# Performance work log

Measured on AMD Instinct MI355X. Metric: run time of the kernel, lower is better.

## Reference

```python
import jax, jax.numpy as jnp
import numpy as np

N_CLUSTER = 1
SIZE, RATIO = 32, 0.1


def _lin_mat(n_in, n_out):
    # bilinear, align_corners=True interpolation matrix [n_out, n_in]
    src = np.arange(n_out) * (n_in - 1) / (n_out - 1)
    lo = np.floor(src).astype(np.int64)
    hi = np.minimum(lo + 1, n_in - 1)
    w = (src - lo).astype(np.float32)
    M = np.zeros((n_out, n_in), np.float32)
    M[np.arange(n_out), lo] += 1.0 - w
    M[np.arange(n_out), hi] += w
    return jnp.asarray(M)


def setup_inputs() -> dict:
    key = jax.random.key(0)
    ks = jax.random.split(key, 5)
    B, D, H, W, C = 16, 128, 128, 128, 6
    inp = {
        "assp": jax.random.normal(ks[0], (B, D, H, W), jnp.float32),
        "cls_w": jax.random.normal(ks[1], (C, D), jnp.float32) * 0.05,
        "cls_b": jnp.zeros((C,), jnp.float32),
        "key_w": jax.random.normal(ks[2], (128, D), jnp.float32) * 0.05,
        "key_b": jnp.zeros((128,), jnp.float32),
        "query_w": jax.random.normal(ks[3], (C, 128, D), jnp.float32) * 0.05,
        "query_b": jnp.zeros((C, 128), jnp.float32),
    }
    rng = np.random.default_rng(0)
    idx = rng.permutation(SIZE * SIZE)[: int(SIZE * SIZE * RATIO)]  # 102 unique pixels
    inp["px"] = jnp.asarray(idx // SIZE, jnp.int32)
    inp["py"] = jnp.asarray(idx % SIZE, jnp.int32)
    return inp


def reference(assp, cls_w, cls_b, key_w, key_b, query_w, query_b, px, py):
    B, D, H, W = assp.shape
    C = cls_w.shape[0]
    # pseudo labels (torch.no_grad)
    feats = jax.lax.stop_gradient(assp)
    pseudo = jnp.einsum('bdhw,cd->bchw', feats, cls_w) + cls_b[None, :, None, None]
    mask = jnp.argmax(pseudo, axis=1)                      # [B,H,W]
    onehot = jax.nn.one_hot(mask, C, dtype=assp.dtype)      # [B,H,W,C]
    counts = onehot.sum((1, 2))                             # [B,C]
    sums = jnp.einsum('bdhw,bhwc->bcd', assp, onehot)       # masked class sums
    protoC = sums / (counts[..., None] + 1e-5)              # [B,C,D]
    protoC = jnp.where(counts[..., None] > 0, protoC, 0.0)  # zero_prototype fallback
    protos12 = jnp.broadcast_to(protoC[:, :, None, :], (B, C, 2, D)).reshape(B, 2 * C, D)

    # DomainTrain: gather sampled pixels, L2 dist to 12 prototypes, argmin, scatter replace
    feat_px = assp[:, :, px, py]                            # [B,D,Np]
    diff = protos12[:, :, None, :] - feat_px.transpose(0, 2, 1)[:, None, :, :]  # [B,12,Np,D]
    dist = jnp.linalg.norm(diff, axis=-1)                   # [B,12,Np]
    closest = jnp.argmin(dist, axis=1)                      # [B,Np]
    repl = jnp.take_along_axis(protos12, closest[..., None], axis=1)  # [B,Np,D]
    assp = assp.at[:, :, px, py].set(repl.transpose(0, 2, 1))
    protos4 = protos12.reshape(B, C, 2, D)

    # key / query attention
    keymap = jnp.einsum('bdhw,kd->bkhw', assp, key_w) + key_b[None, :, None, None]
    q = jnp.einsum('bijd,ikd->bijk', protos4, query_w) + query_b[None, :, None, :]  # [B,C,2,128]
    sim = jnp.einsum('bijk,bkhw->bijhw', q, keymap).reshape(B, 2 * C, H, W)
    simw = jax.nn.softmax(sim / (2 * C) * N_CLUSTER, axis=1).mean(axis=1)  # [B,H,W]

    weighted = assp * simw[:, None]
    x = jnp.einsum('bdhw,cd->bchw', weighted, cls_w) + cls_b[None, :, None, None]
    My = _lin_mat(H, 4 * H)
    Mx = _lin_mat(W, 4 * W)
    xup = jnp.einsum('Hh,bchw,Ww->bcHW', My, x, Mx)
    return xup
```

## Files before the change

### kernel.cpp

```cpp
#include <hip/hip_runtime.h>

namespace {

constexpr int B  = 16;
constexpr int D  = 128;
constexpr int C  = 6;
constexpr int H  = 128;
constexpr int W  = 128;
constexpr int HWC = H * W;
constexpr int HO = 512, WO = 512;
constexpr int TILE = 64;
constexpr int TPB  = 4;

__global__ __launch_bounds__(256) void k_fused(const float* __restrict__ assp,
                                               const float* __restrict__ cls_w,
                                               const float* __restrict__ cls_b,
                                               float* __restrict__ sums,
                                               int* __restrict__ counts,
                                               float* __restrict__ x) {
  __shared__ float tile[D * TILE];
  __shared__ float red[4 * C * TILE];
  __shared__ float ws[C * D];
  __shared__ float bs[C];

  const int t  = threadIdx.x;
  const int b  = blockIdx.y;
  for (int i = t; i < C * D; i += 256) ws[i] = cls_w[i];
  if (t < C) bs[t] = cls_b[t];

  const int lane = t & 63;
  const int wv   = t >> 6;
  const int d2b  = t & 127;
  const int h2b  = t >> 7;
  const int d1   = t >> 5;
  const int px2  = (t & 31) * 2;

  float acc2b[C] = {0.f, 0.f, 0.f, 0.f, 0.f, 0.f};
  int   cnt_run  = 0;

  const int hw_base = blockIdx.x * (TILE * TPB);
  const float* bbase = assp + ((size_t)b * D) * HWC + hw_base;

  float2 v[16];
#pragma unroll
  for (int j = 0; j < 16; ++j) {
    int d = d1 + 8 * j;
    v[j] = *(const float2*)(bbase + (size_t)d * HWC + px2);
  }

  __syncthreads();

  for (int it = 0; it < TPB; ++it) {
    const int hw0 = hw_base + it * TILE;

#pragma unroll
    for (int j = 0; j < 16; ++j) {
      int d = d1 + 8 * j;
      *(float2*)&tile[d * TILE + (px2 ^ (d & 62))] = v[j];
    }
    __syncthreads();

    if (it + 1 < TPB) {
      const float* nbase = bbase + (it + 1) * TILE;
#pragma unroll
      for (int j = 0; j < 16; ++j) {
        int d = d1 + 8 * j;
        v[j] = *(const float2*)(nbase + (size_t)d * HWC + px2);
      }
    }

    {
      float a[C] = {0.f, 0.f, 0.f, 0.f, 0.f, 0.f};
#pragma unroll
      for (int dd = 0; dd < 32; ++dd) {
        int d = wv * 32 + dd;
        float vv = tile[d * TILE + (lane ^ (d & 62))];
#pragma unroll
        for (int c = 0; c < C; ++c) a[c] += vv * ws[c * D + d];
      }
#pragma unroll
      for (int c = 0; c < C; ++c) red[(wv * C + c) * TILE + lane] = a[c];
    }
    __syncthreads();

    int cls;
    {
      float s[C];
#pragma unroll
      for (int c = 0; c < C; ++c)
        s[c] = red[(0 * C + c) * TILE + lane] + red[(1 * C + c) * TILE + lane]
             + red[(2 * C + c) * TILE + lane] + red[(3 * C + c) * TILE + lane];
      float bv = s[0] + bs[0]; cls = 0;
#pragma unroll
      for (int c = 1; c < C; ++c) {
        float pv = s[c] + bs[c];
        if (pv > bv) { bv = pv; cls = c; }
      }
      if (wv == 0) {
        const float inv12 = 1.0f / 12.0f;
        float* xb = x + ((size_t)b * C) * HWC + hw0 + lane;
#pragma unroll
        for (int c = 0; c < C; ++c) xb[(size_t)c * HWC] = s[c] * inv12 + bs[c];
#pragma unroll
        for (int c = 0; c < C; ++c) {
          unsigned long long m = __ballot(cls == c);
          if (lane == c) cnt_run += (int)__popcll(m);
        }
      }
    }

#pragma unroll
    for (int i = 0; i < 32; ++i) {
      int px = h2b * 32 + i;
      float vv = tile[d2b * TILE + (px ^ (d2b & 62))];
      int c = __shfl(cls, px, 64);
#pragma unroll
      for (int cc = 0; cc < C; ++cc) acc2b[cc] += (c == cc) ? vv : 0.f;
    }
    __syncthreads();
  }

  float* part = red;
  if (h2b == 1) {
#pragma unroll
    for (int c = 0; c < C; ++c) part[c * D + d2b] = acc2b[c];
  }
  __syncthreads();
  if (h2b == 0) {
#pragma unroll
    for (int c = 0; c < C; ++c) {
      float s = acc2b[c] + part[c * D + d2b];
      atomicAdd(&sums[((size_t)b * C + c) * D + d2b], s);
    }
  }
  if (wv == 0 && lane < C) atomicAdd(&counts[b * C + lane], cnt_run);
}

__global__ void k_patch(const float* __restrict__ assp,
                        const float* __restrict__ sums,
                        const int* __restrict__ counts,
                        const float* __restrict__ cls_w,
                        const float* __restrict__ cls_b,
                        const int* __restrict__ px,
                        const int* __restrict__ py,
                        int P,
                        float* __restrict__ x) {
  int bp = blockIdx.x;
  int b = bp / P, p = bp % P;
  int hw = px[p] * W + py[p];
  int lane = threadIdx.x;
  const float* fbase = assp + ((size_t)b * D) * HWC + hw;

  float f0 = fbase[(size_t)lane * HWC];
  float f1 = fbase[(size_t)(lane + 64) * HWC];

  float pv0[C], pv1[C], ds[C];
#pragma unroll
  for (int c = 0; c < C; ++c) {
    float cnt = (float)counts[b * C + c];
    float s0 = sums[((size_t)b * C + c) * D + lane];
    float s1 = sums[((size_t)b * C + c) * D + lane + 64];
    float q0 = (cnt > 0.f) ? s0 / (cnt + 1e-5f) : 0.f;
    float q1 = (cnt > 0.f) ? s1 / (cnt + 1e-5f) : 0.f;
    pv0[c] = q0; pv1[c] = q1;
    float e0 = q0 - f0, e1 = q1 - f1;
    float tt = e0 * e0 + e1 * e1;
#pragma unroll
    for (int off = 32; off >= 1; off >>= 1) tt += __shfl_xor(tt, off, 64);
    ds[c] = tt;
  }
  int best = 0; float bv = ds[0];
#pragma unroll
  for (int c = 1; c < C; ++c)
    if (ds[c] < bv) { bv = ds[c]; best = c; }

  float v0 = 0.f, v1 = 0.f;
#pragma unroll
  for (int c = 0; c < C; ++c) {
    if (best == c) { v0 = pv0[c]; v1 = pv1[c]; }
  }

  float myx = 0.f;
#pragma unroll
  for (int c = 0; c < C; ++c) {
    float tt = v0 * cls_w[c * D + lane] + v1 * cls_w[c * D + lane + 64];
#pragma unroll
    for (int off = 32; off >= 1; off >>= 1) tt += __shfl_xor(tt, off, 64);
    float val = tt * (1.0f / 12.0f) + cls_b[c];
    if (lane == c) myx = val;
  }
  if (lane < C) x[((size_t)b * C + lane) * HWC + hw] = myx;
}

__global__ __launch_bounds__(256) void k_up(const float* __restrict__ x,
                                            float* __restrict__ out) {
  __shared__ float rows[3 * W];

  const int t = threadIdx.x;
  const size_t base = (size_t)blockIdx.x * 1024;
  const int bc = (int)(base >> 18);
  const int Y0 = ((int)(base >> 9)) & (HO - 1);

  const int ry = (Y0 * (H - 1)) / (HO - 1);

  if (t < 96) {
    int r  = t >> 5;
    int xx = (t & 31) * 4;
    int rr = ry + r; if (rr > H - 1) rr = H - 1;
    *(float4*)&rows[r * W + xx] =
        *(const float4*)(x + (size_t)bc * HWC + (size_t)rr * W + xx);
  }
  __syncthreads();

  const int h  = t >> 7;
  const int tt = t & 127;
  const int Y  = Y0 + h;

  const int ynum = Y * (H - 1);
  const int yl   = ynum / (HO - 1);
  const float wy = (float)((double)(ynum - yl * (HO - 1)) * (1.0 / (HO - 1)));
  int yh = yl + 1; if (yh > H - 1) yh = H - 1;
  const float* r0 = &rows[(yl - ry) * W];
  const float* r1 = &rows[(yh - ry) * W];

  float o[4];
#pragma unroll
  for (int j = 0; j < 4; ++j) {
    int X   = 4 * tt + j;
    int num = X * (W - 1);
    int lo  = num / (WO - 1);
    float wx = (float)((double)(num - lo * (WO - 1)) * (1.0 / (WO - 1)));
    int hi = lo + 1; if (hi > W - 1) hi = W - 1;

    float v00 = r0[lo], v01 = r0[hi], v10 = r1[lo], v11 = r1[hi];
    o[j] = (1.f - wy) * ((1.f - wx) * v00 + wx * v01)
         +        wy  * ((1.f - wx) * v10 + wx * v11);
  }
  float4 o4 = {o[0], o[1], o[2], o[3]};
  *(float4*)(out + base + (size_t)h * WO + 4 * tt) = o4;
}

}

extern "C" void kernel_launch(void* const* d_in, const int* in_sizes, int n_in,
                              void* d_out, int out_size, void* d_ws, size_t ws_size,
                              hipStream_t stream) {
  const float* assp  = (const float*)d_in[0];
  const float* cls_w = (const float*)d_in[1];
  const float* cls_b = (const float*)d_in[2];
  const int*   px    = (const int*)d_in[7];
  const int*   py    = (const int*)d_in[8];
  const int    P     = in_sizes[7];

  char* ws = (char*)d_ws;
  float* sums   = (float*)ws;
  int*   counts = (int*)(ws + 49152);
  float* x      = (float*)(ws + 65536);

  float* out = (float*)d_out;

  hipMemsetAsync(ws, 0, 49152 + 384, stream);
  k_fused<<<dim3(HWC / (TILE * TPB), B), 256, 0, stream>>>(assp, cls_w, cls_b,
                                                           sums, counts, x);
  k_patch<<<B * P, 64, 0, stream>>>(assp, sums, counts, cls_w, cls_b, px, py, P, x);
  k_up<<<(B * C * HO * WO) / 1024, 256, 0, stream>>>(x, out);
}
```

Baseline: 268.9 us.

## Widen tile loads to float4, read class weights via scalar loads, vectorize LDS reads

Global loads of the assp tile switch from float2 to float4, and the LDS swizzle is changed to keep 16-byte alignment for float4 stores and reads. The shared-memory copy of cls_w and cls_b is removed. Weights are read directly from global memory using a wave-uniform index from readfirstlane, so the compiler can use scalar loads. The masked class-sum loop now reads four pixels per LDS access instead of one, cutting LDS instruction count at the cost of more shuffles per iteration.

New measurement: 295.8 us. 10.0% more time.

```diff
diff --git a/kernel.cpp b/kernel.cpp
--- a/kernel.cpp
+++ b/kernel.cpp
@@ -12,6 +12,10 @@
 constexpr int TILE = 64;
 constexpr int TPB  = 4;
 
+__device__ __forceinline__ int sw(int d, int px) {
+  return px ^ (d & 60) ^ (((d >> 5) & 1) << 4);
+}
+
 __global__ __launch_bounds__(256) void k_fused(const float* __restrict__ assp,
                                                const float* __restrict__ cls_w,
                                                const float* __restrict__ cls_b,
@@ -20,20 +24,16 @@
                                                float* __restrict__ x) {
   __shared__ float tile[D * TILE];
   __shared__ float red[4 * C * TILE];
-  __shared__ float ws[C * D];
-  __shared__ float bs[C];
 
   const int t  = threadIdx.x;
   const int b  = blockIdx.y;
-  for (int i = t; i < C * D; i += 256) ws[i] = cls_w[i];
-  if (t < C) bs[t] = cls_b[t];
-
   const int lane = t & 63;
   const int wv   = t >> 6;
+  const int wvu  = __builtin_amdgcn_readfirstlane(wv);
   const int d2b  = t & 127;
   const int h2b  = t >> 7;
-  const int d1   = t >> 5;
-  const int px2  = (t & 31) * 2;
+  const int sr   = t >> 4;
+  const int spx  = (t & 15) * 4;
 
   float acc2b[C] = {0.f, 0.f, 0.f, 0.f, 0.f, 0.f};
   int   cnt_run  = 0;
@@ -41,45 +41,41 @@
   const int hw_base = blockIdx.x * (TILE * TPB);
   const float* bbase = assp + ((size_t)b * D) * HWC + hw_base;
 
-  float2 v[16];
-#pragma unroll
-  for (int j = 0; j < 16; ++j) {
-    int d = d1 + 8 * j;
-    v[j] = *(const float2*)(bbase + (size_t)d * HWC + px2);
-  }
-
-  __syncthreads();
+  float4 v[8];
+#pragma unroll
+  for (int j = 0; j < 8; ++j)
+    v[j] = *(const float4*)(bbase + (size_t)(sr + 16 * j) * HWC + spx);
+
+  const float* wsr = cls_w + wvu * 32;
 
   for (int it = 0; it < TPB; ++it) {
     const int hw0 = hw_base + it * TILE;
 
 #pragma unroll
-    for (int j = 0; j < 16; ++j) {
-      int d = d1 + 8 * j;
-      *(float2*)&tile[d * TILE + (px2 ^ (d & 62))] = v[j];
+    for (int j = 0; j < 8; ++j) {
+      int d = sr + 16 * j;
+      *(float4*)&tile[d * TILE + sw(d, spx)] = v[j];
     }
     __syncthreads();
 
     if (it + 1 < TPB) {
-      const float* nbase = bbase + (it + 1) * TILE;
-#pragma unroll
-      for (int j = 0; j < 16; ++j) {
-        int d = d1 + 8 * j;
-        v[j] = *(const float2*)(nbase + (size_t)d * HWC + px2);
-      }
+      const float* nb = bbase + (it + 1) * TILE;
+#pragma unroll
+      for (int j = 0; j < 8; ++j)
+        v[j] = *(const float4*)(nb + (size_t)(sr + 16 * j) * HWC + spx);
     }
 
     {
       float a[C] = {0.f, 0.f, 0.f, 0.f, 0.f, 0.f};
 #pragma unroll
       for (int dd = 0; dd < 32; ++dd) {
-        int d = wv * 32 + dd;
-        float vv = tile[d * TILE + (lane ^ (d & 62))];
-#pragma unroll
-        for (int c = 0; c < C; ++c) a[c] += vv * ws[c * D + d];
-      }
-#pragma unroll
-      for (int c = 0; c < C; ++c) red[(wv * C + c) * TILE + lane] = a[c];
+        int d = wvu * 32 + dd;
+        float vv = tile[d * TILE + sw(d, lane)];
+#pragma unroll
+        for (int c = 0; c < C; ++c) a[c] += vv * wsr[c * D + dd];
+      }
+#pragma unroll
+      for (int c = 0; c < C; ++c) red[(wvu * C + c) * TILE + lane] = a[c];
     }
     __syncthreads();
 
@@ -90,17 +86,17 @@
       for (int c = 0; c < C; ++c)
         s[c] = red[(0 * C + c) * TILE + lane] + red[(1 * C + c) * TILE + lane]
              + red[(2 * C + c) * TILE + lane] + red[(3 * C + c) * TILE + lane];
-      float bv = s[0] + bs[0]; cls = 0;
+      float bv = s[0] + cls_b[0]; cls = 0;
 #pragma unroll
       for (int c = 1; c < C; ++c) {
-        float pv = s[c] + bs[c];
+        float pv = s[c] + cls_b[c];
         if (pv > bv) { bv = pv; cls = c; }
       }
       if (wv == 0) {
         const float inv12 = 1.0f / 12.0f;
         float* xb = x + ((size_t)b * C) * HWC + hw0 + lane;
 #pragma unroll
-        for (int c = 0; c < C; ++c) xb[(size_t)c * HWC] = s[c] * inv12 + bs[c];
+        for (int c = 0; c < C; ++c) xb[(size_t)c * HWC] = s[c] * inv12 + cls_b[c];
 #pragma unroll
         for (int c = 0; c < C; ++c) {
           unsigned long long m = __ballot(cls == c);
@@ -110,12 +106,20 @@
     }
 
 #pragma unroll
-    for (int i = 0; i < 32; ++i) {
-      int px = h2b * 32 + i;
-      float vv = tile[d2b * TILE + (px ^ (d2b & 62))];
-      int c = __shfl(cls, px, 64);
-#pragma unroll
-      for (int cc = 0; cc < C; ++cc) acc2b[cc] += (c == cc) ? vv : 0.f;
+    for (int i = 0; i < 8; ++i) {
+      int px4 = h2b * 32 + 4 * i;
+      float4 u = *(const float4*)&tile[d2b * TILE + sw(d2b, px4)];
+      int c0 = __shfl(cls, px4 + 0, 64);
+      int c1 = __shfl(cls, px4 + 1, 64);
+      int c2 = __shfl(cls, px4 + 2, 64);
+      int c3 = __shfl(cls, px4 + 3, 64);
+#pragma unroll
+      for (int cc = 0; cc < C; ++cc) {
+        acc2b[cc] += (c0 == cc) ? u.x : 0.f;
+        acc2b[cc] += (c1 == cc) ? u.y : 0.f;
+        acc2b[cc] += (c2 == cc) ? u.z : 0.f;
+        acc2b[cc] += (c3 == cc) ? u.w : 0.f;
+      }
     }
     __syncthreads();
   }
```

## Split fused classify/sum kernel into separate classify and masked-sum passes

Applied to the files above, without the earlier changes.

Replaces the single LDS-tiled kernel, which computed argmax labels and per-class feature sums in one pass, with two kernels. The first computes the class logits per pixel straight from global memory and writes a byte mask plus counts. The second re-reads the features alongside the mask to build the per-class sums. This removes shared-memory tiling, swizzling and barriers, but reads the 128 MB input twice and adds a mask buffer round trip.

Result: slower. 279.9 us (+4.1%).

```diff
diff --git a/kernel.cpp b/kernel.cpp
--- a/kernel.cpp
+++ b/kernel.cpp
@@ -9,131 +9,89 @@
 constexpr int W  = 128;
 constexpr int HWC = H * W;
 constexpr int HO = 512, WO = 512;
-constexpr int TILE = 64;
-constexpr int TPB  = 4;
-
-__global__ __launch_bounds__(256) void k_fused(const float* __restrict__ assp,
-                                               const float* __restrict__ cls_w,
-                                               const float* __restrict__ cls_b,
-                                               float* __restrict__ sums,
-                                               int* __restrict__ counts,
-                                               float* __restrict__ x) {
-  __shared__ float tile[D * TILE];
-  __shared__ float red[4 * C * TILE];
-  __shared__ float ws[C * D];
-  __shared__ float bs[C];
+constexpr int CHUNK = 2048;
+
+__global__ __launch_bounds__(256) void k_cls(const float* __restrict__ assp,
+                                             const float* __restrict__ cls_w,
+                                             const float* __restrict__ cls_b,
+                                             float* __restrict__ x,
+                                             unsigned char* __restrict__ mask,
+                                             int* __restrict__ counts) {
+  __shared__ int csh[4 * C];
 
   const int t  = threadIdx.x;
   const int b  = blockIdx.y;
-  for (int i = t; i < C * D; i += 256) ws[i] = cls_w[i];
-  if (t < C) bs[t] = cls_b[t];
-
+  const int px = blockIdx.x * 256 + t;
   const int lane = t & 63;
   const int wv   = t >> 6;
-  const int d2b  = t & 127;
-  const int h2b  = t >> 7;
-  const int d1   = t >> 5;
-  const int px2  = (t & 31) * 2;
-
-  float acc2b[C] = {0.f, 0.f, 0.f, 0.f, 0.f, 0.f};
-  int   cnt_run  = 0;
-
-  const int hw_base = blockIdx.x * (TILE * TPB);
-  const float* bbase = assp + ((size_t)b * D) * HWC + hw_base;
-
-  float2 v[16];
-#pragma unroll
-  for (int j = 0; j < 16; ++j) {
-    int d = d1 + 8 * j;
-    v[j] = *(const float2*)(bbase + (size_t)d * HWC + px2);
-  }
-
+
+  const float* col = assp + ((size_t)b * D) * HWC + px;
+
+  float a[C] = {0.f, 0.f, 0.f, 0.f, 0.f, 0.f};
+#pragma unroll 8
+  for (int d = 0; d < D; ++d) {
+    float vv = col[(size_t)d * HWC];
+#pragma unroll
+    for (int c = 0; c < C; ++c) a[c] += vv * cls_w[c * D + d];
+  }
+
+  float bv = a[0] + cls_b[0];
+  int cls = 0;
+#pragma unroll
+  for (int c = 1; c < C; ++c) {
+    float pv = a[c] + cls_b[c];
+    if (pv > bv) { bv = pv; cls = c; }
+  }
+
+  const float inv12 = 1.0f / 12.0f;
+  float* xb = x + ((size_t)b * C) * HWC + px;
+#pragma unroll
+  for (int c = 0; c < C; ++c) xb[(size_t)c * HWC] = a[c] * inv12 + cls_b[c];
+
+  mask[(size_t)b * HWC + px] = (unsigned char)cls;
+
+#pragma unroll
+  for (int c = 0; c < C; ++c) {
+    unsigned long long m = __ballot(cls == c);
+    if (lane == 0) csh[wv * C + c] = (int)__popcll(m);
+  }
   __syncthreads();
-
-  for (int it = 0; it < TPB; ++it) {
-    const int hw0 = hw_base + it * TILE;
-
-#pragma unroll
-    for (int j = 0; j < 16; ++j) {
-      int d = d1 + 8 * j;
-      *(float2*)&tile[d * TILE + (px2 ^ (d & 62))] = v[j];
-    }
-    __syncthreads();
-
-    if (it + 1 < TPB) {
-      const float* nbase = bbase + (it + 1) * TILE;
-#pragma unroll
-      for (int j = 0; j < 16; ++j) {
-        int d = d1 + 8 * j;
-        v[j] = *(const float2*)(nbase + (size_t)d * HWC + px2);
-      }
-    }
-
-    {
-      float a[C] = {0.f, 0.f, 0.f, 0.f, 0.f, 0.f};
-#pragma unroll
-      for (int dd = 0; dd < 32; ++dd) {
-        int d = wv * 32 + dd;
-        float vv = tile[d * TILE + (lane ^ (d & 62))];
-#pragma unroll
-        for (int c = 0; c < C; ++c) a[c] += vv * ws[c * D + d];
-      }
-#pragma unroll
-      for (int c = 0; c < C; ++c) red[(wv * C + c) * TILE + lane] = a[c];
-    }
-    __syncthreads();
-
-    int cls;
-    {
-      float s[C];
-#pragma unroll
-      for (int c = 0; c < C; ++c)
-        s[c] = red[(0 * C + c) * TILE + lane] + red[(1 * C + c) * TILE + lane]
-             + red[(2 * C + c) * TILE + lane] + red[(3 * C + c) * TILE + lane];
-      float bv = s[0] + bs[0]; cls = 0;
-#pragma unroll
-      for (int c = 1; c < C; ++c) {
-        float pv = s[c] + bs[c];
-        if (pv > bv) { bv = pv; cls = c; }
-      }
-      if (wv == 0) {
-        const float inv12 = 1.0f / 12.0f;
-        float* xb = x + ((size_t)b * C) * HWC + hw0 + lane;
-#pragma unroll
-        for (int c = 0; c < C; ++c) xb[(size_t)c * HWC] = s[c] * inv12 + bs[c];
-#pragma unroll
-        for (int c = 0; c < C; ++c) {
-          unsigned long long m = __ballot(cls == c);
-          if (lane == c) cnt_run += (int)__popcll(m);
-        }
-      }
-    }
-
-#pragma unroll
-    for (int i = 0; i < 32; ++i) {
-      int px = h2b * 32 + i;
-      float vv = tile[d2b * TILE + (px ^ (d2b & 62))];
-      int c = __shfl(cls, px, 64);
-#pragma unroll
-      for (int cc = 0; cc < C; ++cc) acc2b[cc] += (c == cc) ? vv : 0.f;
-    }
-    __syncthreads();
-  }
-
-  float* part = red;
-  if (h2b == 1) {
-#pragma unroll
-    for (int c = 0; c < C; ++c) part[c * D + d2b] = acc2b[c];
-  }
-  __syncthreads();
-  if (h2b == 0) {
-#pragma unroll
-    for (int c = 0; c < C; ++c) {
-      float s = acc2b[c] + part[c * D + d2b];
-      atomicAdd(&sums[((size_t)b * C + c) * D + d2b], s);
-    }
-  }
-  if (wv == 0 && lane < C) atomicAdd(&counts[b * C + lane], cnt_run);
+  if (t < C)
+    atomicAdd(&counts[b * C + t],
+              csh[0 * C + t] + csh[1 * C + t] + csh[2 * C + t] + csh[3 * C + t]);
+}
+
+__global__ __launch_bounds__(256) void k_sum(const float* __restrict__ assp,
+                                             const unsigned char* __restrict__ mask,
+                                             float* __restrict__ sums) {
+  const int t    = threadIdx.x;
+  const int lane = t & 63;
+  const int wv   = t >> 6;
+  const int b    = blockIdx.z;
+  const int d    = blockIdx.y * 4 + wv;
+  const int px0  = blockIdx.x * CHUNK;
+
+  const float* row = assp + ((size_t)b * D + d) * HWC + px0;
+  const unsigned char* mrow = mask + (size_t)b * HWC + px0;
+
+  float acc[C] = {0.f, 0.f, 0.f, 0.f, 0.f, 0.f};
+#pragma unroll 4
+  for (int i = 0; i < CHUNK / 64; ++i) {
+    float vv = row[i * 64 + lane];
+    int   c  = mrow[i * 64 + lane];
+#pragma unroll
+    for (int cc = 0; cc < C; ++cc) acc[cc] += (c == cc) ? vv : 0.f;
+  }
+
+  float out = 0.f;
+#pragma unroll
+  for (int cc = 0; cc < C; ++cc) {
+    float s = acc[cc];
+#pragma unroll
+    for (int off = 32; off >= 1; off >>= 1) s += __shfl_xor(s, off, 64);
+    if (lane == cc) out = s;
+  }
+  if (lane < C) atomicAdd(&sums[((size_t)b * C + lane) * D + d], out);
 }
 
 __global__ void k_patch(const float* __restrict__ assp,
@@ -253,15 +211,16 @@
   const int    P     = in_sizes[7];
 
   char* ws = (char*)d_ws;
-  float* sums   = (float*)ws;
-  int*   counts = (int*)(ws + 49152);
-  float* x      = (float*)(ws + 65536);
+  float* sums            = (float*)ws;
+  int*   counts          = (int*)(ws + 49152);
+  float* x               = (float*)(ws + 65536);
+  unsigned char* maskbuf = (unsigned char*)(ws + 8388608);
 
   float* out = (float*)d_out;
 
   hipMemsetAsync(ws, 0, 49152 + 384, stream);
-  k_fused<<<dim3(HWC / (TILE * TPB), B), 256, 0, stream>>>(assp, cls_w, cls_b,
-                                                           sums, counts, x);
+  k_cls<<<dim3(HWC / 256, B), 256, 0, stream>>>(assp, cls_w, cls_b, x, maskbuf, counts);
+  k_sum<<<dim3(HWC / CHUNK, D / 4, B), 256, 0, stream>>>(assp, maskbuf, sums);
   k_patch<<<B * P, 64, 0, stream>>>(assp, sums, counts, cls_w, cls_b, px, py, P, x);
   k_up<<<(B * C * HO * WO) / 1024, 256, 0, stream>>>(x, out);
 }
```
